# Kernel optimization log

Hardware: AMD Instinct MI355X
Metric: run time of the kernel (lower is better)

Reference implementation:

```python
import jax, jax.numpy as jnp
import numpy as np

EPSILON = 1e-6
SEARCH_RADIUS = 11 // 2  # search_window_size=11 -> 121 shifts
PATCH_RADIUS = 5 // 2    # patch_size=5 box sum


def shift_stack(t, r):
    # Matches ShiftStack: outer loop x_shift, inner loop y_shift, roll dims (H,W)=(2,3).
    # t: [B,C,H,W] -> [B,C,H,W,(2r+1)^2]
    return jnp.stack(
        [jnp.roll(t, (dy, dx), axis=(2, 3))
         for dx in range(-r, r + 1) for dy in range(-r, r + 1)],
        axis=-1,
    )


def box_sum(t, r):
    # Circular box-filter sum over a (2r+1)x(2r+1) window; separable form is
    # mathematically identical to the original 25 rolls (rolls commute/add).
    s = sum(jnp.roll(t, d, axis=2) for d in range(-r, r + 1))
    return sum(jnp.roll(s, d, axis=3) for d in range(-r, r + 1))


def setup_inputs() -> dict:
    key = jax.random.key(0)
    k1, k2 = jax.random.split(key)
    rgb = jax.random.uniform(k1, (1, 3, 512, 512), dtype=jnp.float32)
    # realistic noise std in [0.02, 0.12]
    sigma = jax.random.uniform(k2, (1, 1, 1, 1), dtype=jnp.float32) * 0.1 + 0.02
    return {"rgb": rgb, "sigma": sigma}


def reference(rgb, sigma):
    h = sigma * 2.0                                     # [B,1,1,1]
    y = 0.299 * rgb[:, :1] + 0.587 * rgb[:, 1:2] + 0.114 * rgb[:, 2:]  # [B,1,H,W]
    rgb_stack = shift_stack(rgb, SEARCH_RADIUS)         # [B,3,H,W,K]
    y_stack = shift_stack(y, SEARCH_RADIUS)             # [B,1,H,W,K]
    sq_diff = (y[..., None] - y_stack) ** 2             # [B,1,H,W,K]
    distances = jnp.sqrt(box_sum(sq_diff, PATCH_RADIUS))
    weights = jnp.exp(-distances / (jax.nn.relu(h)[..., None] + EPSILON))  # [B,1,H,W,K]
    denoised = (weights * rgb_stack).sum(axis=-1) / weights.sum(axis=-1)   # [B,3,H,W]
    return jnp.clip(denoised, 0.0, 1.0)
```

## Files before the change

### kernel.cpp

```cpp
#include <hip/hip_runtime.h>
#include <math.h>

#define IH 512
#define IW 512
#define NPX (IH*IW)

#define TW 60
#define BH 8
#define NXT 9
#define YROWS 22
#define YCOLS 74
#define YSZ2 (YROWS*YCOLS)

#define TS 32
#define YHALO 7
#define RHALO 5
#define YD (TS + 2*YHALO)
#define RD (TS + 2*RHALO)
#define RSZ (RD*RD)
#define MYSZ (YD*YD)

#define FSQRT(x) __builtin_amdgcn_sqrtf(x)
#if __has_builtin(__builtin_amdgcn_exp2f)
#define FEXP2(x) __builtin_amdgcn_exp2f(x)
#else
#define FEXP2(x) exp2f(x)
#endif

__device__ __forceinline__ float dpp_shl1(float x) {
    return __int_as_float(__builtin_amdgcn_update_dpp(
        0, __float_as_int(x), 0x130, 0xf, 0xf, true));
}

__global__ __launch_bounds__(256)
void nlm_part(const float* __restrict__ rgb,
              const float* __restrict__ sigma,
              float4* __restrict__ ws) {
    __shared__ float YL[YSZ2];

    const int tid   = threadIdx.x;
    const int lane  = tid & 63;
    const int wavei = tid >> 6;
    const int tx0 = blockIdx.x * TW;
    const int ty0 = blockIdx.y * BH;
    const int slice = blockIdx.z;

    const float* Rp = rgb;
    const float* Gp = rgb + NPX;
    const float* Bp = rgb + 2*NPX;

    for (int idx = tid; idx < YSZ2; idx += 256) {
        int a = idx / YCOLS, b = idx - a*YCOLS;
        int gy = (ty0 + a - 7) & (IH-1);
        int gx = (tx0 + b - 7) & (IW-1);
        int g = gy*IW + gx;
        YL[idx] = 0.299f*Rp[g] + 0.587f*Gp[g] + 0.114f*Bp[g];
    }
    __syncthreads();

    const float m2 = -1.4426950408889634f /
                     (fmaxf(sigma[0]*2.0f, 0.0f) + 1e-6f);

    const int l  = lane;
    const int r0 = wavei*2;

    float yb6[6];
    #pragma unroll
    for (int i = 0; i < 6; ++i)
        yb6[i] = YL[(r0+5+i)*YCOLS + (l+5)];

    float accR[2]={0,0}, accG[2]={0,0}, accB[2]={0,0}, den[2]={0,0};

    const int dxlo  = (slice == 0) ? -5 : (slice == 1 ? -1 : 3);
    const int dxcnt = (slice == 2) ? 3 : 4;

    for (int u = 0; u < dxcnt; ++u) {
        const int dx = dxlo + u;
        const int ysb  = r0*YCOLS + (l + 5 - dx);
        const int coli = (tx0 + l - dx) & (IW-1);

        float sub6[6];
        #pragma unroll
        for (int j = 0; j < 6; ++j)
            sub6[j] = YL[ysb + j*YCOLS];

        float rw[2], gw[2], bw[2];
        int oP = (((ty0 + r0 - 5) & (IH-1)) << 9) + coli;
        rw[0] = Rp[oP]; gw[0] = Gp[oP]; bw[0] = Bp[oP];
        oP = (oP + IW) & (NPX-1);

        #pragma unroll
        for (int k = 0; k <= 10; ++k) {
            rw[(k+1)&1] = Rp[oP];
            gw[(k+1)&1] = Gp[oP];
            bw[(k+1)&1] = Bp[oP];
            oP = (oP + IW) & (NPX-1);
            if (k > 0)
                sub6[(k+5)%6] = YL[ysb + (k+5)*YCOLS];

            float pre[7]; pre[0] = 0.f;
            #pragma unroll
            for (int i = 0; i < 6; ++i) {
                float d = yb6[i] - sub6[(i+k)%6];
                pre[i+1] = fmaf(d, d, pre[i]);
            }
            float V[2];
            V[0] = pre[5] - pre[0];
            V[1] = pre[6] - pre[1];

            float box[2];
            #pragma unroll
            for (int rr = 0; rr < 2; ++rr) {
                float s1 = dpp_shl1(V[rr]);
                float s2 = dpp_shl1(s1);
                float s3 = dpp_shl1(s2);
                float s4 = dpp_shl1(s3);
                box[rr] = ((V[rr] + s1) + (s2 + s3)) + s4;
            }
            #pragma unroll
            for (int rr = 0; rr < 2; ++rr) {
                float w = FEXP2(FSQRT(fmaxf(box[rr], 0.f)) * m2);
                accR[rr] = fmaf(w, rw[(k+rr)&1], accR[rr]);
                accG[rr] = fmaf(w, gw[(k+rr)&1], accG[rr]);
                accB[rr] = fmaf(w, bw[(k+rr)&1], accB[rr]);
                den[rr] += w;
            }
        }
    }

    if (l < TW && tx0 + l < IW) {
        #pragma unroll
        for (int rr = 0; rr < 2; ++rr) {
            int px = (ty0 + r0 + rr)*IW + tx0 + l;
            ws[(size_t)slice*NPX + px] =
                make_float4(accR[rr], accG[rr], accB[rr], den[rr]);
        }
    }
}

__global__ __launch_bounds__(256)
void nlm_combine(const float4* __restrict__ ws, float* __restrict__ out) {
    int px = blockIdx.x * 256 + threadIdx.x;
    float4 a = ws[px];
    float4 b = ws[NPX + px];
    float4 c = ws[2*(size_t)NPX + px];
    float r  = (a.x + b.x) + c.x;
    float g  = (a.y + b.y) + c.y;
    float bl = (a.z + b.z) + c.z;
    float w  = (a.w + b.w) + c.w;
    float iw = 1.0f / w;
    out[px]           = fminf(fmaxf(r  * iw, 0.f), 1.f);
    out[NPX + px]     = fminf(fmaxf(g  * iw, 0.f), 1.f);
    out[2*NPX + px]   = fminf(fmaxf(bl * iw, 0.f), 1.f);
}

__global__ __launch_bounds__(256)
void nlm_mono(const float* __restrict__ rgb,
              const float* __restrict__ sigma,
              float* __restrict__ out) {
    __shared__ float Y[MYSZ];
    __shared__ float RGBL[3 * RSZ];

    const int tid = threadIdx.x;
    const int tx0 = blockIdx.x * TS;
    const int ty0 = blockIdx.y * TS;

    const float* Rp = rgb;
    const float* Gp = rgb + NPX;
    const float* Bp = rgb + 2 * NPX;

    for (int idx = tid; idx < MYSZ; idx += 256) {
        int a = idx / YD, b = idx - a * YD;
        int gy = (ty0 + a - YHALO) & (IH - 1);
        int gx = (tx0 + b - YHALO) & (IW - 1);
        int g = gy * IW + gx;
        Y[idx] = 0.299f * Rp[g] + 0.587f * Gp[g] + 0.114f * Bp[g];
    }
    for (int idx = tid; idx < RSZ; idx += 256) {
        int a = idx / RD, b = idx - a * RD;
        int gy = (ty0 + a - RHALO) & (IH - 1);
        int gx = (tx0 + b - RHALO) & (IW - 1);
        int g = gy * IW + gx;
        RGBL[idx]           = Rp[g];
        RGBL[RSZ + idx]     = Gp[g];
        RGBL[2 * RSZ + idx] = Bp[g];
    }
    __syncthreads();

    const float minv_h = -1.0f / (fmaxf(sigma[0] * 2.0f, 0.0f) + 1e-6f);
    const int tx = tid & 31;
    const int tz = tid >> 5;
    const int r0 = tz * 4;

    const int ybase = (YHALO + r0 - 2) * YD + (YHALO + tx - 2);
    float yb[8][5];
    #pragma unroll
    for (int i = 0; i < 8; ++i)
        #pragma unroll
        for (int b = 0; b < 5; ++b)
            yb[i][b] = Y[ybase + i * YD + b];

    float accR[4] = {0.f,0.f,0.f,0.f}, accG[4] = {0.f,0.f,0.f,0.f};
    float accB[4] = {0.f,0.f,0.f,0.f}, den[4] = {0.f,0.f,0.f,0.f};

    for (int dx = -5; dx <= 5; ++dx) {
        const int ybd = (YHALO + r0 - 7) * YD + (YHALO + tx - 2 - dx);
        const int rbd = (RHALO + r0 - 5) * RD + (RHALO + tx - dx);

        #pragma unroll
        for (int k = 0; k <= 10; ++k) {
            float hs[8];
            #pragma unroll
            for (int i = 0; i < 8; ++i) {
                float s = 0.f;
                #pragma unroll
                for (int b = 0; b < 5; ++b) {
                    float d = yb[i][b] - Y[ybd + (i + k) * YD + b];
                    s = fmaf(d, d, s);
                }
                hs[i] = s;
            }
            float pre[9];
            pre[0] = 0.f;
            #pragma unroll
            for (int i = 0; i < 8; ++i) pre[i + 1] = pre[i] + hs[i];
            #pragma unroll
            for (int rr = 0; rr < 4; ++rr) {
                float box = pre[rr + 5] - pre[rr];
                float w = __expf(FSQRT(box) * minv_h);
                const int s2 = rbd + (rr + k) * RD;
                accR[rr] = fmaf(w, RGBL[s2], accR[rr]);
                accG[rr] = fmaf(w, RGBL[RSZ + s2], accG[rr]);
                accB[rr] = fmaf(w, RGBL[2 * RSZ + s2], accB[rr]);
                den[rr] += w;
            }
        }
    }

    #pragma unroll
    for (int rr = 0; rr < 4; ++rr) {
        int px = (ty0 + r0 + rr) * IW + tx0 + tx;
        float iw = 1.0f / den[rr];
        out[px]           = fminf(fmaxf(accR[rr] * iw, 0.f), 1.f);
        out[NPX + px]     = fminf(fmaxf(accG[rr] * iw, 0.f), 1.f);
        out[2 * NPX + px] = fminf(fmaxf(accB[rr] * iw, 0.f), 1.f);
    }
}

extern "C" void kernel_launch(void* const* d_in, const int* in_sizes, int n_in,
                              void* d_out, int out_size, void* d_ws, size_t ws_size,
                              hipStream_t stream) {
    const float* rgb   = (const float*)d_in[0];
    const float* sigma = (const float*)d_in[1];
    float* out = (float*)d_out;

    const size_t need = (size_t)3 * NPX * sizeof(float4);
    if (ws_size >= need) {
        float4* ws = (float4*)d_ws;
        dim3 grid(NXT, IH / BH, 3);
        nlm_part<<<grid, dim3(256), 0, stream>>>(rgb, sigma, ws);
        nlm_combine<<<dim3(NPX / 256), dim3(256), 0, stream>>>(ws, out);
    } else {
        dim3 grid(IW / TS, IH / TS);
        nlm_mono<<<grid, dim3(256), 0, stream>>>(rgb, sigma, out);
    }
}
```

Baseline: 35.70 us.

## Fuse dx-sliced partial kernel and combine pass into one single-pass kernel

The search-window shifts are no longer split into three dx slices. Each block now loops over all 11 horizontal shifts and normalizes and writes the clipped output directly. This removes the float4 workspace write, the separate combine kernel and its extra launch. In exchange the grid shrinks threefold, to 576 blocks on a 256-CU device, so occupancy and latency hiding drop and the tail may be uneven. The unused fallback mono kernel is also deleted.

```diff
diff --git a/kernel.cpp b/kernel.cpp
--- a/kernel.cpp
+++ b/kernel.cpp
@@ -12,14 +12,6 @@
 #define YCOLS 74
 #define YSZ2 (YROWS*YCOLS)
 
-#define TS 32
-#define YHALO 7
-#define RHALO 5
-#define YD (TS + 2*YHALO)
-#define RD (TS + 2*RHALO)
-#define RSZ (RD*RD)
-#define MYSZ (YD*YD)
-
 #define FSQRT(x) __builtin_amdgcn_sqrtf(x)
 #if __has_builtin(__builtin_amdgcn_exp2f)
 #define FEXP2(x) __builtin_amdgcn_exp2f(x)
@@ -33,9 +25,9 @@
 }
 
 __global__ __launch_bounds__(256)
-void nlm_part(const float* __restrict__ rgb,
-              const float* __restrict__ sigma,
-              float4* __restrict__ ws) {
+void nlm_mono2(const float* __restrict__ rgb,
+               const float* __restrict__ sigma,
+               float* __restrict__ out) {
     __shared__ float YL[YSZ2];
 
     const int tid   = threadIdx.x;
@@ -43,7 +35,6 @@
     const int wavei = tid >> 6;
     const int tx0 = blockIdx.x * TW;
     const int ty0 = blockIdx.y * BH;
-    const int slice = blockIdx.z;
 
     const float* Rp = rgb;
     const float* Gp = rgb + NPX;
@@ -71,11 +62,7 @@
 
     float accR[2]={0,0}, accG[2]={0,0}, accB[2]={0,0}, den[2]={0,0};
 
-    const int dxlo  = (slice == 0) ? -5 : (slice == 1 ? -1 : 3);
-    const int dxcnt = (slice == 2) ? 3 : 4;
-
-    for (int u = 0; u < dxcnt; ++u) {
-        const int dx = dxlo + u;
+    for (int dx = -5; dx <= 5; ++dx) {
         const int ysb  = r0*YCOLS + (l + 5 - dx);
         const int coli = (tx0 + l - dx) & (IW-1);
 
@@ -132,118 +119,11 @@
         #pragma unroll
         for (int rr = 0; rr < 2; ++rr) {
             int px = (ty0 + r0 + rr)*IW + tx0 + l;
-            ws[(size_t)slice*NPX + px] =
-                make_float4(accR[rr], accG[rr], accB[rr], den[rr]);
+            float iw = 1.0f / den[rr];
+            out[px]           = fminf(fmaxf(accR[rr] * iw, 0.f), 1.f);
+            out[NPX + px]     = fminf(fmaxf(accG[rr] * iw, 0.f), 1.f);
+            out[2*NPX + px]   = fminf(fmaxf(accB[rr] * iw, 0.f), 1.f);
         }
-    }
-}
-
-__global__ __launch_bounds__(256)
-void nlm_combine(const float4* __restrict__ ws, float* __restrict__ out) {
-    int px = blockIdx.x * 256 + threadIdx.x;
-    float4 a = ws[px];
-    float4 b = ws[NPX + px];
-    float4 c = ws[2*(size_t)NPX + px];
-    float r  = (a.x + b.x) + c.x;
-    float g  = (a.y + b.y) + c.y;
-    float bl = (a.z + b.z) + c.z;
-    float w  = (a.w + b.w) + c.w;
-    float iw = 1.0f / w;
-    out[px]           = fminf(fmaxf(r  * iw, 0.f), 1.f);
-    out[NPX + px]     = fminf(fmaxf(g  * iw, 0.f), 1.f);
-    out[2*NPX + px]   = fminf(fmaxf(bl * iw, 0.f), 1.f);
-}
-
-__global__ __launch_bounds__(256)
-void nlm_mono(const float* __restrict__ rgb,
-              const float* __restrict__ sigma,
-              float* __restrict__ out) {
-    __shared__ float Y[MYSZ];
-    __shared__ float RGBL[3 * RSZ];
-
-    const int tid = threadIdx.x;
-    const int tx0 = blockIdx.x * TS;
-    const int ty0 = blockIdx.y * TS;
-
-    const float* Rp = rgb;
-    const float* Gp = rgb + NPX;
-    const float* Bp = rgb + 2 * NPX;
-
-    for (int idx = tid; idx < MYSZ; idx += 256) {
-        int a = idx / YD, b = idx - a * YD;
-        int gy = (ty0 + a - YHALO) & (IH - 1);
-        int gx = (tx0 + b - YHALO) & (IW - 1);
-        int g = gy * IW + gx;
-        Y[idx] = 0.299f * Rp[g] + 0.587f * Gp[g] + 0.114f * Bp[g];
-    }
-    for (int idx = tid; idx < RSZ; idx += 256) {
-        int a = idx / RD, b = idx - a * RD;
-        int gy = (ty0 + a - RHALO) & (IH - 1);
-        int gx = (tx0 + b - RHALO) & (IW - 1);
-        int g = gy * IW + gx;
-        RGBL[idx]           = Rp[g];
-        RGBL[RSZ + idx]     = Gp[g];
-        RGBL[2 * RSZ + idx] = Bp[g];
-    }
-    __syncthreads();
-
-    const float minv_h = -1.0f / (fmaxf(sigma[0] * 2.0f, 0.0f) + 1e-6f);
-    const int tx = tid & 31;
-    const int tz = tid >> 5;
-    const int r0 = tz * 4;
-
-    const int ybase = (YHALO + r0 - 2) * YD + (YHALO + tx - 2);
-    float yb[8][5];
-    #pragma unroll
-    for (int i = 0; i < 8; ++i)
-        #pragma unroll
-        for (int b = 0; b < 5; ++b)
-            yb[i][b] = Y[ybase + i * YD + b];
-
-    float accR[4] = {0.f,0.f,0.f,0.f}, accG[4] = {0.f,0.f,0.f,0.f};
-    float accB[4] = {0.f,0.f,0.f,0.f}, den[4] = {0.f,0.f,0.f,0.f};
-
-    for (int dx = -5; dx <= 5; ++dx) {
-        const int ybd = (YHALO + r0 - 7) * YD + (YHALO + tx - 2 - dx);
-        const int rbd = (RHALO + r0 - 5) * RD + (RHALO + tx - dx);
-
-        #pragma unroll
-        for (int k = 0; k <= 10; ++k) {
-            float hs[8];
-            #pragma unroll
-            for (int i = 0; i < 8; ++i) {
-                float s = 0.f;
-                #pragma unroll
-                for (int b = 0; b < 5; ++b) {
-                    float d = yb[i][b] - Y[ybd + (i + k) * YD + b];
-                    s = fmaf(d, d, s);
-                }
-                hs[i] = s;
-            }
-            float pre[9];
-            pre[0] = 0.f;
-            #pragma unroll
-            for (int i = 0; i < 8; ++i) pre[i + 1] = pre[i] + hs[i];
-            #pragma unroll
-            for (int rr = 0; rr < 4; ++rr) {
-                float box = pre[rr + 5] - pre[rr];
-                float w = __expf(FSQRT(box) * minv_h);
-                const int s2 = rbd + (rr + k) * RD;
-                accR[rr] = fmaf(w, RGBL[s2], accR[rr]);
-                accG[rr] = fmaf(w, RGBL[RSZ + s2], accG[rr]);
-                accB[rr] = fmaf(w, RGBL[2 * RSZ + s2], accB[rr]);
-                den[rr] += w;
-            }
-        }
-    }
-
-    #pragma unroll
-    for (int rr = 0; rr < 4; ++rr) {
-        int px = (ty0 + r0 + rr) * IW + tx0 + tx;
-        float iw = 1.0f / den[rr];
-        out[px]           = fminf(fmaxf(accR[rr] * iw, 0.f), 1.f);
-        out[NPX + px]     = fminf(fmaxf(accG[rr] * iw, 0.f), 1.f);
-        out[2 * NPX + px] = fminf(fmaxf(accB[rr] * iw, 0.f), 1.f);
     }
 }
 
@@ -254,14 +134,6 @@
     const float* sigma = (const float*)d_in[1];
     float* out = (float*)d_out;
 
-    const size_t need = (size_t)3 * NPX * sizeof(float4);
-    if (ws_size >= need) {
-        float4* ws = (float4*)d_ws;
-        dim3 grid(NXT, IH / BH, 3);
-        nlm_part<<<grid, dim3(256), 0, stream>>>(rgb, sigma, ws);
-        nlm_combine<<<dim3(NPX / 256), dim3(256), 0, stream>>>(ws, out);
-    } else {
-        dim3 grid(IW / TS, IH / TS);
-        nlm_mono<<<grid, dim3(256), 0, stream>>>(rgb, sigma, out);
-    }
+    dim3 grid(NXT, IH / BH);
+    nlm_mono2<<<grid, dim3(256), 0, stream>>>(rgb, sigma, out);
 }
```

After: 38.95 us. 9.1% more time.
